# Performance work log

Hardware: AMD Instinct MI355X
Metric: run time of the kernel (lower is better)

The kernel has to match this reference:

```python
import jax, jax.numpy as jnp
import numpy as np

H = 64   # hidden_size
I = 4    # input_size
O = 1    # output_size

def setup_inputs() -> dict:
    key = jax.random.key(0)
    ks = jax.random.split(key, 7)
    B, T = 1024, 1024
    s = 1.0 / np.sqrt(H)
    x = jax.random.normal(ks[0], (B, T, I), dtype=jnp.float32)
    # PyTorch nn.LSTM params, gate order (i, f, g, o)
    W_ih = jax.random.uniform(ks[1], (4 * H, I), minval=-s, maxval=s, dtype=jnp.float32)
    W_hh = jax.random.uniform(ks[2], (4 * H, H), minval=-s, maxval=s, dtype=jnp.float32)
    b_ih = jax.random.uniform(ks[3], (4 * H,), minval=-s, maxval=s, dtype=jnp.float32)
    b_hh = jax.random.uniform(ks[4], (4 * H,), minval=-s, maxval=s, dtype=jnp.float32)
    W_fc = jax.random.uniform(ks[5], (O, H), minval=-s, maxval=s, dtype=jnp.float32)
    b_fc = jax.random.uniform(ks[6], (O,), minval=-s, maxval=s, dtype=jnp.float32)
    return {"x": x, "W_ih": W_ih, "W_hh": W_hh, "b_ih": b_ih, "b_hh": b_hh,
            "W_fc": W_fc, "b_fc": b_fc}

def _lstm(x, W_ih, W_hh, b_ih, b_hh):
    B, T, _ = x.shape
    # precompute input contribution for all timesteps: [T, B, 4H]
    xg = (jnp.einsum('bti,gi->btg', x, W_ih) + b_ih + b_hh).transpose(1, 0, 2)

    def step(carry, xt):
        h, c = carry
        g = xt + h @ W_hh.T                     # [B, 4H]
        i, f, gg, o = jnp.split(g, 4, axis=-1)  # torch gate order i,f,g,o
        i = jax.nn.sigmoid(i)
        f = jax.nn.sigmoid(f)
        gg = jnp.tanh(gg)
        o = jax.nn.sigmoid(o)
        c = f * c + i * gg
        h = o * jnp.tanh(c)
        return (h, c), h

    h0 = jnp.zeros((B, H), dtype=x.dtype)
    c0 = jnp.zeros((B, H), dtype=x.dtype)
    _, hs = jax.lax.scan(step, (h0, c0), xg)    # hs: [T, B, H]
    return hs.transpose(1, 0, 2)                # [B, T, H]

def reference(x, W_ih, W_hh, b_ih, b_hh, W_fc, b_fc):
    out = _lstm(x, W_ih, W_hh, b_ih, b_hh)      # [B, T, H]
    # dropout in eval mode == identity (deterministic reference)
    return out @ W_fc.T + b_fc                  # [B, T, 1]
```

## Files before the change

### kernel.cpp

```cpp
#include <hip/hip_runtime.h>

#define TLEN  1024
#define HN    64
#define LOG2E 1.4426950408889634f

typedef __fp16 half2v __attribute__((ext_vector_type(2)));
typedef __fp16 half8v __attribute__((ext_vector_type(8)));
typedef float  float4v __attribute__((ext_vector_type(4)));


#define FOR16(X) \
    X(0) X(1) X(2) X(3) X(4) X(5) X(6) X(7) \
    X(8) X(9) X(10) X(11) X(12) X(13) X(14) X(15)

__global__ __launch_bounds__(64, 1)
void lstm_mfma2(const float* __restrict__ x,
                const float* __restrict__ W_ih,
                const float* __restrict__ W_hh,
                const float* __restrict__ b_ih,
                const float* __restrict__ b_hh,
                const float* __restrict__ W_fc,
                const float* __restrict__ b_fc,
                float* __restrict__ out)
{
    const int b   = blockIdx.x;
    const int l   = threadIdx.x;
    const int col = l & 15;
    const int rg  = l >> 4;

    __shared__ float ring[64][65];
    __shared__ alignas(16) unsigned short hbuf[HN];

    hbuf[l] = 0;

#define DECLW(t) half8v wb##t##_0, wb##t##_1;
    FOR16(DECLW)
#undef DECLW

#define LOADW(t) { \
    const float sc = (((t) >> 2) == 2) ? (2.0f * LOG2E) : LOG2E; \
    const float* wr = W_hh + ((t) * 16 + col) * HN + rg * 8; \
    wb##t##_0[0] = (__fp16)(wr[0] * sc);  wb##t##_0[1] = (__fp16)(wr[1] * sc); \
    wb##t##_0[2] = (__fp16)(wr[2] * sc);  wb##t##_0[3] = (__fp16)(wr[3] * sc); \
    wb##t##_0[4] = (__fp16)(wr[4] * sc);  wb##t##_0[5] = (__fp16)(wr[5] * sc); \
    wb##t##_0[6] = (__fp16)(wr[6] * sc);  wb##t##_0[7] = (__fp16)(wr[7] * sc); \
    wb##t##_1[0] = (__fp16)(wr[32] * sc); wb##t##_1[1] = (__fp16)(wr[33] * sc); \
    wb##t##_1[2] = (__fp16)(wr[34] * sc); wb##t##_1[3] = (__fp16)(wr[35] * sc); \
    wb##t##_1[4] = (__fp16)(wr[36] * sc); wb##t##_1[5] = (__fp16)(wr[37] * sc); \
    wb##t##_1[6] = (__fp16)(wr[38] * sc); wb##t##_1[7] = (__fp16)(wr[39] * sc); \
    asm volatile("" : "+v"(wb##t##_0), "+v"(wb##t##_1)); }
    FOR16(LOADW)
#undef LOADW

    half2v wip0 = __builtin_amdgcn_cvt_pkrtz(W_ih[(0 * HN + l) * 4 + 0] * LOG2E,
                                             W_ih[(0 * HN + l) * 4 + 1] * LOG2E);
    half2v wip1 = __builtin_amdgcn_cvt_pkrtz(W_ih[(0 * HN + l) * 4 + 2] * LOG2E,
                                             W_ih[(0 * HN + l) * 4 + 3] * LOG2E);
    half2v wfp0 = __builtin_amdgcn_cvt_pkrtz(W_ih[(1 * HN + l) * 4 + 0] * LOG2E,
                                             W_ih[(1 * HN + l) * 4 + 1] * LOG2E);
    half2v wfp1 = __builtin_amdgcn_cvt_pkrtz(W_ih[(1 * HN + l) * 4 + 2] * LOG2E,
                                             W_ih[(1 * HN + l) * 4 + 3] * LOG2E);
    half2v wgp0 = __builtin_amdgcn_cvt_pkrtz(W_ih[(2 * HN + l) * 4 + 0] * 2.0f * LOG2E,
                                             W_ih[(2 * HN + l) * 4 + 1] * 2.0f * LOG2E);
    half2v wgp1 = __builtin_amdgcn_cvt_pkrtz(W_ih[(2 * HN + l) * 4 + 2] * 2.0f * LOG2E,
                                             W_ih[(2 * HN + l) * 4 + 3] * 2.0f * LOG2E);
    half2v wop0 = __builtin_amdgcn_cvt_pkrtz(W_ih[(3 * HN + l) * 4 + 0] * LOG2E,
                                             W_ih[(3 * HN + l) * 4 + 1] * LOG2E);
    half2v wop1 = __builtin_amdgcn_cvt_pkrtz(W_ih[(3 * HN + l) * 4 + 2] * LOG2E,
                                             W_ih[(3 * HN + l) * 4 + 3] * LOG2E);

    const float bias_i = (b_ih[0 * HN + l] + b_hh[0 * HN + l]) * LOG2E;
    const float bias_f = (b_ih[1 * HN + l] + b_hh[1 * HN + l]) * LOG2E;
    const float bias_g = (b_ih[2 * HN + l] + b_hh[2 * HN + l]) * (2.0f * LOG2E);
    const float bias_o = (b_ih[3 * HN + l] + b_hh[3 * HN + l]) * LOG2E;
    const float wfc = W_fc[l];
    const float bfc = b_fc[0];

    const bool rb0 = (rg & 1) != 0;
    const bool rb1 = (rg & 2) != 0;

    const float* xb = x   + (size_t)b * TLEN * 4;
    float*       ob = out + (size_t)b * TLEN;

    float h = 0.0f, c = 0.0f;
    const float4v zf = {0.0f, 0.0f, 0.0f, 0.0f};

    float4 xcur = *(const float4*)(xb + (size_t)l * 4);

    for (int ci = 0; ci < TLEN / 64; ++ci) {
        const int cn = (ci < TLEN / 64 - 1) ? ci + 1 : ci;
        float4 xnext = *(const float4*)(xb + (size_t)(cn * 64 + l) * 4);

        const int xq0 = __builtin_bit_cast(int, __builtin_amdgcn_cvt_pkrtz(xcur.x, xcur.y));
        const int xq1 = __builtin_bit_cast(int, __builtin_amdgcn_cvt_pkrtz(xcur.z, xcur.w));

        for (int s = 0; s < 64; ++s) {
            const half8v a0 = *(const half8v*)&hbuf[rg * 8];
            const half8v a1 = *(const half8v*)&hbuf[32 + rg * 8];

            const int xi0 = __builtin_amdgcn_readlane(xq0, s);
            const int xi1 = __builtin_amdgcn_readlane(xq1, s);
            const half2v xh0 = __builtin_bit_cast(half2v, xi0);
            const half2v xh1 = __builtin_bit_cast(half2v, xi1);

            float ai = __builtin_amdgcn_fdot2(wip0, xh0, bias_i, false);
            float af = __builtin_amdgcn_fdot2(wfp0, xh0, bias_f, false);
            float ag = __builtin_amdgcn_fdot2(wgp0, xh0, bias_g, false);
            float ao = __builtin_amdgcn_fdot2(wop0, xh0, bias_o, false);
            ai = __builtin_amdgcn_fdot2(wip1, xh1, ai, false);
            af = __builtin_amdgcn_fdot2(wfp1, xh1, af, false);
            ag = __builtin_amdgcn_fdot2(wgp1, xh1, ag, false);
            ao = __builtin_amdgcn_fdot2(wop1, xh1, ao, false);

#define MM(t) \
            float4v d##t = __builtin_amdgcn_mfma_f32_16x16x32_f16(a0, wb##t##_0, zf, 0, 0, 0); \
            d##t = __builtin_amdgcn_mfma_f32_16x16x32_f16(a1, wb##t##_1, d##t, 0, 0, 0);
            FOR16(MM)
#undef MM

            {
                const float i01 = rb0 ? d1[0]  : d0[0];
                const float i23 = rb0 ? d3[0]  : d2[0];
                ai += rb1 ? i23 : i01;
                const float f01 = rb0 ? d5[0]  : d4[0];
                const float f23 = rb0 ? d7[0]  : d6[0];
                af += rb1 ? f23 : f01;
                const float g01 = rb0 ? d9[0]  : d8[0];
                const float g23 = rb0 ? d11[0] : d10[0];
                ag += rb1 ? g23 : g01;
                const float o01 = rb0 ? d13[0] : d12[0];
                const float o23 = rb0 ? d15[0] : d14[0];
                ao += rb1 ? o23 : o01;
            }

            float si = __builtin_amdgcn_rcpf(1.0f + __builtin_amdgcn_exp2f(-ai));
            float sf = __builtin_amdgcn_rcpf(1.0f + __builtin_amdgcn_exp2f(-af));
            float tg = 1.0f - 2.0f * __builtin_amdgcn_rcpf(
                                         1.0f + __builtin_amdgcn_exp2f(ag));
            float so = __builtin_amdgcn_rcpf(1.0f + __builtin_amdgcn_exp2f(-ao));

            c = sf * c + si * tg;
            float th = 1.0f - 2.0f * __builtin_amdgcn_rcpf(
                           1.0f + __builtin_amdgcn_exp2f(c * (2.0f * LOG2E)));
            h = so * th;

            const int hpk = __builtin_bit_cast(int,
                                __builtin_amdgcn_cvt_pkrtz(h, h));
            hbuf[l] = (unsigned short)(hpk & 0xffff);
            ring[s][l] = h * wfc;
        }

        __syncthreads();
        float s0 = 0.f, s1 = 0.f, s2 = 0.f, s3 = 0.f;
#pragma unroll
        for (int k = 0; k < HN; k += 4) {
            s0 += ring[l][k];
            s1 += ring[l][k + 1];
            s2 += ring[l][k + 2];
            s3 += ring[l][k + 3];
        }
        ob[ci * 64 + l] = (s0 + s1) + (s2 + s3) + bfc;

        xcur = xnext;
    }
}

extern "C" void kernel_launch(void* const* d_in, const int* in_sizes, int n_in,
                              void* d_out, int out_size, void* d_ws, size_t ws_size,
                              hipStream_t stream) {
    const float* x    = (const float*)d_in[0];
    const float* W_ih = (const float*)d_in[1];
    const float* W_hh = (const float*)d_in[2];
    const float* b_ih = (const float*)d_in[3];
    const float* b_hh = (const float*)d_in[4];
    const float* W_fc = (const float*)d_in[5];
    const float* b_fc = (const float*)d_in[6];
    float* out = (float*)d_out;

    const int B = in_sizes[0] / (TLEN * 4);
    lstm_mfma2<<<dim3(B), dim3(64), 0, stream>>>(
        x, W_ih, W_hh, b_ih, b_hh, W_fc, b_fc, out);
}
```

Baseline: 525.8 us.

## Split recurrent matvec between MFMA for i,f gates and VALU dot2 for g,o

Halves the per-step MFMA count by computing only the input and forget gate recurrent products with matrix instructions, while the cell and output gate products are done per lane with packed fp16 dot2 instructions over the whole hidden vector read from LDS. The goal is to overlap matrix-unit and vector-ALU work on the serial per-step critical path. In exchange it adds 64 extra VGPRs of packed weights, eight broadcast LDS reads per step and 64 dot2 instructions per lane per step.

```diff
diff --git a/kernel.cpp b/kernel.cpp
--- a/kernel.cpp
+++ b/kernel.cpp
@@ -9,19 +9,22 @@
 typedef float  float4v __attribute__((ext_vector_type(4)));
 
 
-#define FOR16(X) \
+#define FOR8(X)  X(0) X(1) X(2) X(3) X(4) X(5) X(6) X(7)
+#define FOR32(X) \
     X(0) X(1) X(2) X(3) X(4) X(5) X(6) X(7) \
-    X(8) X(9) X(10) X(11) X(12) X(13) X(14) X(15)
+    X(8) X(9) X(10) X(11) X(12) X(13) X(14) X(15) \
+    X(16) X(17) X(18) X(19) X(20) X(21) X(22) X(23) \
+    X(24) X(25) X(26) X(27) X(28) X(29) X(30) X(31)
 
 __global__ __launch_bounds__(64, 1)
-void lstm_mfma2(const float* __restrict__ x,
-                const float* __restrict__ W_ih,
-                const float* __restrict__ W_hh,
-                const float* __restrict__ b_ih,
-                const float* __restrict__ b_hh,
-                const float* __restrict__ W_fc,
-                const float* __restrict__ b_fc,
-                float* __restrict__ out)
+void lstm_dual(const float* __restrict__ x,
+               const float* __restrict__ W_ih,
+               const float* __restrict__ W_hh,
+               const float* __restrict__ b_ih,
+               const float* __restrict__ b_hh,
+               const float* __restrict__ W_fc,
+               const float* __restrict__ b_fc,
+               float* __restrict__ out)
 {
     const int b   = blockIdx.x;
     const int l   = threadIdx.x;
@@ -34,23 +37,36 @@
     hbuf[l] = 0;
 
 #define DECLW(t) half8v wb##t##_0, wb##t##_1;
-    FOR16(DECLW)
+    FOR8(DECLW)
 #undef DECLW
 
 #define LOADW(t) { \
-    const float sc = (((t) >> 2) == 2) ? (2.0f * LOG2E) : LOG2E; \
     const float* wr = W_hh + ((t) * 16 + col) * HN + rg * 8; \
-    wb##t##_0[0] = (__fp16)(wr[0] * sc);  wb##t##_0[1] = (__fp16)(wr[1] * sc); \
-    wb##t##_0[2] = (__fp16)(wr[2] * sc);  wb##t##_0[3] = (__fp16)(wr[3] * sc); \
-    wb##t##_0[4] = (__fp16)(wr[4] * sc);  wb##t##_0[5] = (__fp16)(wr[5] * sc); \
-    wb##t##_0[6] = (__fp16)(wr[6] * sc);  wb##t##_0[7] = (__fp16)(wr[7] * sc); \
-    wb##t##_1[0] = (__fp16)(wr[32] * sc); wb##t##_1[1] = (__fp16)(wr[33] * sc); \
-    wb##t##_1[2] = (__fp16)(wr[34] * sc); wb##t##_1[3] = (__fp16)(wr[35] * sc); \
-    wb##t##_1[4] = (__fp16)(wr[36] * sc); wb##t##_1[5] = (__fp16)(wr[37] * sc); \
-    wb##t##_1[6] = (__fp16)(wr[38] * sc); wb##t##_1[7] = (__fp16)(wr[39] * sc); \
+    wb##t##_0[0] = (__fp16)(wr[0] * LOG2E);  wb##t##_0[1] = (__fp16)(wr[1] * LOG2E); \
+    wb##t##_0[2] = (__fp16)(wr[2] * LOG2E);  wb##t##_0[3] = (__fp16)(wr[3] * LOG2E); \
+    wb##t##_0[4] = (__fp16)(wr[4] * LOG2E);  wb##t##_0[5] = (__fp16)(wr[5] * LOG2E); \
+    wb##t##_0[6] = (__fp16)(wr[6] * LOG2E);  wb##t##_0[7] = (__fp16)(wr[7] * LOG2E); \
+    wb##t##_1[0] = (__fp16)(wr[32] * LOG2E); wb##t##_1[1] = (__fp16)(wr[33] * LOG2E); \
+    wb##t##_1[2] = (__fp16)(wr[34] * LOG2E); wb##t##_1[3] = (__fp16)(wr[35] * LOG2E); \
+    wb##t##_1[4] = (__fp16)(wr[36] * LOG2E); wb##t##_1[5] = (__fp16)(wr[37] * LOG2E); \
+    wb##t##_1[6] = (__fp16)(wr[38] * LOG2E); wb##t##_1[7] = (__fp16)(wr[39] * LOG2E); \
     asm volatile("" : "+v"(wb##t##_0), "+v"(wb##t##_1)); }
-    FOR16(LOADW)
+    FOR8(LOADW)
 #undef LOADW
+
+    const float* wr_g = W_hh + (2 * HN + l) * HN;
+    const float* wr_o = W_hh + (3 * HN + l) * HN;
+#define DECLP(P) half2v pg##P, po##P;
+    FOR32(DECLP)
+#undef DECLP
+#define LOADP(P) \
+    pg##P = __builtin_amdgcn_cvt_pkrtz(wr_g[2 * (P)] * (2.0f * LOG2E), \
+                                       wr_g[2 * (P) + 1] * (2.0f * LOG2E)); \
+    po##P = __builtin_amdgcn_cvt_pkrtz(wr_o[2 * (P)] * LOG2E, \
+                                       wr_o[2 * (P) + 1] * LOG2E); \
+    asm volatile("" : "+v"(pg##P), "+v"(po##P));
+    FOR32(LOADP)
+#undef LOADP
 
     half2v wip0 = __builtin_amdgcn_cvt_pkrtz(W_ih[(0 * HN + l) * 4 + 0] * LOG2E,
                                              W_ih[(0 * HN + l) * 4 + 1] * LOG2E);
@@ -97,6 +113,20 @@
         for (int s = 0; s < 64; ++s) {
             const half8v a0 = *(const half8v*)&hbuf[rg * 8];
             const half8v a1 = *(const half8v*)&hbuf[32 + rg * 8];
+            const uint4 q0 = *(const uint4*)&hbuf[0];
+            const uint4 q1 = *(const uint4*)&hbuf[8];
+            const uint4 q2 = *(const uint4*)&hbuf[16];
+            const uint4 q3 = *(const uint4*)&hbuf[24];
+            const uint4 q4 = *(const uint4*)&hbuf[32];
+            const uint4 q5 = *(const uint4*)&hbuf[40];
+            const uint4 q6 = *(const uint4*)&hbuf[48];
+            const uint4 q7 = *(const uint4*)&hbuf[56];
+
+#define MM(t) \
+            float4v d##t = __builtin_amdgcn_mfma_f32_16x16x32_f16(a0, wb##t##_0, zf, 0, 0, 0); \
+            d##t = __builtin_amdgcn_mfma_f32_16x16x32_f16(a1, wb##t##_1, d##t, 0, 0, 0);
+            FOR8(MM)
+#undef MM
 
             const int xi0 = __builtin_amdgcn_readlane(xq0, s);
             const int xi1 = __builtin_amdgcn_readlane(xq1, s);
@@ -105,32 +135,46 @@
 
             float ai = __builtin_amdgcn_fdot2(wip0, xh0, bias_i, false);
             float af = __builtin_amdgcn_fdot2(wfp0, xh0, bias_f, false);
-            float ag = __builtin_amdgcn_fdot2(wgp0, xh0, bias_g, false);
-            float ao = __builtin_amdgcn_fdot2(wop0, xh0, bias_o, false);
+            float agE = __builtin_amdgcn_fdot2(wgp0, xh0, bias_g, false);
+            float aoE = __builtin_amdgcn_fdot2(wop0, xh0, bias_o, false);
             ai = __builtin_amdgcn_fdot2(wip1, xh1, ai, false);
             af = __builtin_amdgcn_fdot2(wfp1, xh1, af, false);
-            ag = __builtin_amdgcn_fdot2(wgp1, xh1, ag, false);
-            ao = __builtin_amdgcn_fdot2(wop1, xh1, ao, false);
-
-#define MM(t) \
-            float4v d##t = __builtin_amdgcn_mfma_f32_16x16x32_f16(a0, wb##t##_0, zf, 0, 0, 0); \
-            d##t = __builtin_amdgcn_mfma_f32_16x16x32_f16(a1, wb##t##_1, d##t, 0, 0, 0);
-            FOR16(MM)
-#undef MM
+            agE = __builtin_amdgcn_fdot2(wgp1, xh1, agE, false);
+            aoE = __builtin_amdgcn_fdot2(wop1, xh1, aoE, false);
+            float agO = 0.0f, aoO = 0.0f;
+
+#define GOB(q, P0, P1, P2, P3, AG, AO) { \
+            const half2v hA = __builtin_bit_cast(half2v, (int)(q).x); \
+            const half2v hB = __builtin_bit_cast(half2v, (int)(q).y); \
+            const half2v hC = __builtin_bit_cast(half2v, (int)(q).z); \
+            const half2v hD = __builtin_bit_cast(half2v, (int)(q).w); \
+            AG = __builtin_amdgcn_fdot2(pg##P0, hA, AG, false); \
+            AO = __builtin_amdgcn_fdot2(po##P0, hA, AO, false); \
+            AG = __builtin_amdgcn_fdot2(pg##P1, hB, AG, false); \
+            AO = __builtin_amdgcn_fdot2(po##P1, hB, AO, false); \
+            AG = __builtin_amdgcn_fdot2(pg##P2, hC, AG, false); \
+            AO = __builtin_amdgcn_fdot2(po##P2, hC, AO, false); \
+            AG = __builtin_amdgcn_fdot2(pg##P3, hD, AG, false); \
+            AO = __builtin_amdgcn_fdot2(po##P3, hD, AO, false); }
+            GOB(q0, 0, 1, 2, 3,     agE, aoE)
+            GOB(q4, 16, 17, 18, 19, agO, aoO)
+            GOB(q1, 4, 5, 6, 7,     agE, aoE)
+            GOB(q5, 20, 21, 22, 23, agO, aoO)
+            GOB(q2, 8, 9, 10, 11,   agE, aoE)
+            GOB(q6, 24, 25, 26, 27, agO, aoO)
+            GOB(q3, 12, 13, 14, 15, agE, aoE)
+            GOB(q7, 28, 29, 30, 31, agO, aoO)
+#undef GOB
+            const float ag = agE + agO;
+            const float ao = aoE + aoO;
 
             {
-                const float i01 = rb0 ? d1[0]  : d0[0];
-                const float i23 = rb0 ? d3[0]  : d2[0];
+                const float i01 = rb0 ? d1[0] : d0[0];
+                const float i23 = rb0 ? d3[0] : d2[0];
                 ai += rb1 ? i23 : i01;
-                const float f01 = rb0 ? d5[0]  : d4[0];
-                const float f23 = rb0 ? d7[0]  : d6[0];
+                const float f01 = rb0 ? d5[0] : d4[0];
+                const float f23 = rb0 ? d7[0] : d6[0];
                 af += rb1 ? f23 : f01;
-                const float g01 = rb0 ? d9[0]  : d8[0];
-                const float g23 = rb0 ? d11[0] : d10[0];
-                ag += rb1 ? g23 : g01;
-                const float o01 = rb0 ? d13[0] : d12[0];
-                const float o23 = rb0 ? d15[0] : d14[0];
-                ao += rb1 ? o23 : o01;
             }
 
             float si = __builtin_amdgcn_rcpf(1.0f + __builtin_amdgcn_exp2f(-ai));
@@ -178,6 +222,6 @@
     float* out = (float*)d_out;
 
     const int B = in_sizes[0] / (TLEN * 4);
-    lstm_mfma2<<<dim3(B), dim3(64), 0, stream>>>(
+    lstm_dual<<<dim3(B), dim3(64), 0, stream>>>(
         x, W_ih, W_hh, b_ih, b_hh, W_fc, b_fc, out);
 }
```

New measurement: 596.9 us. 1.14x slower.

## Pack four batch sequences per wavefront using distinct MFMA rows

Applied to the files above, without the earlier changes.

Each 64-lane block now processes four batch elements instead of one. Each element's hidden state sits in its own group of MFMA A-matrix rows, so the recurrent matmul no longer repeats the same row 16 times. Each lane now computes gates and cell state for four hidden units, and the input projection is staged through shared memory per 16-step chunk. The output reduction is rewritten for the new layout and gets an extra barrier. The grid shrinks fourfold, which cuts total MFMA work but puts four times the activation math on each step's serial path. It may also leave many SIMDs idle.

```diff
diff --git a/kernel.cpp b/kernel.cpp
--- a/kernel.cpp
+++ b/kernel.cpp
@@ -12,31 +12,32 @@
 #define FOR16(X) \
     X(0) X(1) X(2) X(3) X(4) X(5) X(6) X(7) \
     X(8) X(9) X(10) X(11) X(12) X(13) X(14) X(15)
+#define FORC(X) X(0) X(1) X(2) X(3)
 
 __global__ __launch_bounds__(64, 1)
-void lstm_mfma2(const float* __restrict__ x,
-                const float* __restrict__ W_ih,
-                const float* __restrict__ W_hh,
-                const float* __restrict__ b_ih,
-                const float* __restrict__ b_hh,
-                const float* __restrict__ W_fc,
-                const float* __restrict__ b_fc,
-                float* __restrict__ out)
+void lstm_e4(const float* __restrict__ x,
+             const float* __restrict__ W_ih,
+             const float* __restrict__ W_hh,
+             const float* __restrict__ b_ih,
+             const float* __restrict__ b_hh,
+             const float* __restrict__ W_fc,
+             const float* __restrict__ b_fc,
+             float* __restrict__ out)
 {
-    const int b   = blockIdx.x;
+    const int b0  = blockIdx.x * 4;
     const int l   = threadIdx.x;
     const int col = l & 15;
     const int rg  = l >> 4;
 
-    __shared__ float ring[64][65];
-    __shared__ alignas(16) unsigned short hbuf[HN];
+    __shared__ alignas(16) unsigned short hbuf[4 * 88];
+    __shared__ alignas(16) unsigned int   xbuf[4 * 34];
+    __shared__ alignas(16) float          ring[16 * 80];
 
-    hbuf[l] = 0;
+    for (int i = l; i < 4 * 88; i += 64) hbuf[i] = 0;
 
 #define DECLW(t) half8v wb##t##_0, wb##t##_1;
     FOR16(DECLW)
 #undef DECLW
-
 #define LOADW(t) { \
     const float sc = (((t) >> 2) == 2) ? (2.0f * LOG2E) : LOG2E; \
     const float* wr = W_hh + ((t) * 16 + col) * HN + rg * 8; \
@@ -52,114 +53,112 @@
     FOR16(LOADW)
 #undef LOADW
 
-    half2v wip0 = __builtin_amdgcn_cvt_pkrtz(W_ih[(0 * HN + l) * 4 + 0] * LOG2E,
-                                             W_ih[(0 * HN + l) * 4 + 1] * LOG2E);
-    half2v wip1 = __builtin_amdgcn_cvt_pkrtz(W_ih[(0 * HN + l) * 4 + 2] * LOG2E,
-                                             W_ih[(0 * HN + l) * 4 + 3] * LOG2E);
-    half2v wfp0 = __builtin_amdgcn_cvt_pkrtz(W_ih[(1 * HN + l) * 4 + 0] * LOG2E,
-                                             W_ih[(1 * HN + l) * 4 + 1] * LOG2E);
-    half2v wfp1 = __builtin_amdgcn_cvt_pkrtz(W_ih[(1 * HN + l) * 4 + 2] * LOG2E,
-                                             W_ih[(1 * HN + l) * 4 + 3] * LOG2E);
-    half2v wgp0 = __builtin_amdgcn_cvt_pkrtz(W_ih[(2 * HN + l) * 4 + 0] * 2.0f * LOG2E,
-                                             W_ih[(2 * HN + l) * 4 + 1] * 2.0f * LOG2E);
-    half2v wgp1 = __builtin_amdgcn_cvt_pkrtz(W_ih[(2 * HN + l) * 4 + 2] * 2.0f * LOG2E,
-                                             W_ih[(2 * HN + l) * 4 + 3] * 2.0f * LOG2E);
-    half2v wop0 = __builtin_amdgcn_cvt_pkrtz(W_ih[(3 * HN + l) * 4 + 0] * LOG2E,
-                                             W_ih[(3 * HN + l) * 4 + 1] * LOG2E);
-    half2v wop1 = __builtin_amdgcn_cvt_pkrtz(W_ih[(3 * HN + l) * 4 + 2] * LOG2E,
-                                             W_ih[(3 * HN + l) * 4 + 3] * LOG2E);
+#define DECLX(c) \
+    half2v wxi##c##a, wxi##c##b, wxf##c##a, wxf##c##b; \
+    half2v wxg##c##a, wxg##c##b, wxo##c##a, wxo##c##b; \
+    float bi##c, bf##c, bg##c, bo##c, wq##c; float cst##c = 0.0f;
+    FORC(DECLX)
+#undef DECLX
+#define LOADX(c) { \
+    const int u = (c) * 16 + col; \
+    wxi##c##a = __builtin_amdgcn_cvt_pkrtz(W_ih[(0*HN+u)*4+0]*LOG2E, W_ih[(0*HN+u)*4+1]*LOG2E); \
+    wxi##c##b = __builtin_amdgcn_cvt_pkrtz(W_ih[(0*HN+u)*4+2]*LOG2E, W_ih[(0*HN+u)*4+3]*LOG2E); \
+    wxf##c##a = __builtin_amdgcn_cvt_pkrtz(W_ih[(1*HN+u)*4+0]*LOG2E, W_ih[(1*HN+u)*4+1]*LOG2E); \
+    wxf##c##b = __builtin_amdgcn_cvt_pkrtz(W_ih[(1*HN+u)*4+2]*LOG2E, W_ih[(1*HN+u)*4+3]*LOG2E); \
+    wxg##c##a = __builtin_amdgcn_cvt_pkrtz(W_ih[(2*HN+u)*4+0]*2.0f*LOG2E, W_ih[(2*HN+u)*4+1]*2.0f*LOG2E); \
+    wxg##c##b = __builtin_amdgcn_cvt_pkrtz(W_ih[(2*HN+u)*4+2]*2.0f*LOG2E, W_ih[(2*HN+u)*4+3]*2.0f*LOG2E); \
+    wxo##c##a = __builtin_amdgcn_cvt_pkrtz(W_ih[(3*HN+u)*4+0]*LOG2E, W_ih[(3*HN+u)*4+1]*LOG2E); \
+    wxo##c##b = __builtin_amdgcn_cvt_pkrtz(W_ih[(3*HN+u)*4+2]*LOG2E, W_ih[(3*HN+u)*4+3]*LOG2E); \
+    bi##c = (b_ih[0*HN+u] + b_hh[0*HN+u]) * LOG2E; \
+    bf##c = (b_ih[1*HN+u] + b_hh[1*HN+u]) * LOG2E; \
+    bg##c = (b_ih[2*HN+u] + b_hh[2*HN+u]) * (2.0f*LOG2E); \
+    bo##c = (b_ih[3*HN+u] + b_hh[3*HN+u]) * LOG2E; \
+    wq##c = W_fc[u]; }
+    FORC(LOADX)
+#undef LOADX
 
-    const float bias_i = (b_ih[0 * HN + l] + b_hh[0 * HN + l]) * LOG2E;
-    const float bias_f = (b_ih[1 * HN + l] + b_hh[1 * HN + l]) * LOG2E;
-    const float bias_g = (b_ih[2 * HN + l] + b_hh[2 * HN + l]) * (2.0f * LOG2E);
-    const float bias_o = (b_ih[3 * HN + l] + b_hh[3 * HN + l]) * LOG2E;
-    const float wfc = W_fc[l];
     const float bfc = b_fc[0];
+    const int   ea  = col >> 2;
 
-    const bool rb0 = (rg & 1) != 0;
-    const bool rb1 = (rg & 2) != 0;
+    float4 xcur = *(const float4*)(x + ((size_t)(b0 + rg) * TLEN + col) * 4);
 
-    const float* xb = x   + (size_t)b * TLEN * 4;
-    float*       ob = out + (size_t)b * TLEN;
+    for (int ci = 0; ci < TLEN / 16; ++ci) {
+        const unsigned xi0 = (unsigned)__builtin_bit_cast(int,
+                                 __builtin_amdgcn_cvt_pkrtz(xcur.x, xcur.y));
+        const unsigned xi1 = (unsigned)__builtin_bit_cast(int,
+                                 __builtin_amdgcn_cvt_pkrtz(xcur.z, xcur.w));
+        *(uint2*)&xbuf[rg * 34 + col * 2] = make_uint2(xi0, xi1);
 
-    float h = 0.0f, c = 0.0f;
-    const float4v zf = {0.0f, 0.0f, 0.0f, 0.0f};
+        const int cn = (ci < TLEN / 16 - 1) ? ci + 1 : ci;
+        float4 xnext = *(const float4*)(x + ((size_t)(b0 + rg) * TLEN
+                                             + cn * 16 + col) * 4);
 
-    float4 xcur = *(const float4*)(xb + (size_t)l * 4);
+        for (int s = 0; s < 16; ++s) {
+            const half8v a0 = *(const half8v*)&hbuf[ea * 88 + rg * 8];
+            const half8v a1 = *(const half8v*)&hbuf[ea * 88 + 32 + rg * 8];
+            const uint2 xw = *(const uint2*)&xbuf[rg * 34 + s * 2];
+            const half2v xh0 = __builtin_bit_cast(half2v, (int)xw.x);
+            const half2v xh1 = __builtin_bit_cast(half2v, (int)xw.y);
 
-    for (int ci = 0; ci < TLEN / 64; ++ci) {
-        const int cn = (ci < TLEN / 64 - 1) ? ci + 1 : ci;
-        float4 xnext = *(const float4*)(xb + (size_t)(cn * 64 + l) * 4);
+#define XDOT(c) \
+            float ai##c = __builtin_amdgcn_fdot2(wxi##c##a, xh0, bi##c, false); \
+            float af##c = __builtin_amdgcn_fdot2(wxf##c##a, xh0, bf##c, false); \
+            float ag##c = __builtin_amdgcn_fdot2(wxg##c##a, xh0, bg##c, false); \
+            float ao##c = __builtin_amdgcn_fdot2(wxo##c##a, xh0, bo##c, false); \
+            ai##c = __builtin_amdgcn_fdot2(wxi##c##b, xh1, ai##c, false); \
+            af##c = __builtin_amdgcn_fdot2(wxf##c##b, xh1, af##c, false); \
+            ag##c = __builtin_amdgcn_fdot2(wxg##c##b, xh1, ag##c, false); \
+            ao##c = __builtin_amdgcn_fdot2(wxo##c##b, xh1, ao##c, false);
+            FORC(XDOT)
+#undef XDOT
 
-        const int xq0 = __builtin_bit_cast(int, __builtin_amdgcn_cvt_pkrtz(xcur.x, xcur.y));
-        const int xq1 = __builtin_bit_cast(int, __builtin_amdgcn_cvt_pkrtz(xcur.z, xcur.w));
-
-        for (int s = 0; s < 64; ++s) {
-            const half8v a0 = *(const half8v*)&hbuf[rg * 8];
-            const half8v a1 = *(const half8v*)&hbuf[32 + rg * 8];
-
-            const int xi0 = __builtin_amdgcn_readlane(xq0, s);
-            const int xi1 = __builtin_amdgcn_readlane(xq1, s);
-            const half2v xh0 = __builtin_bit_cast(half2v, xi0);
-            const half2v xh1 = __builtin_bit_cast(half2v, xi1);
-
-            float ai = __builtin_amdgcn_fdot2(wip0, xh0, bias_i, false);
-            float af = __builtin_amdgcn_fdot2(wfp0, xh0, bias_f, false);
-            float ag = __builtin_amdgcn_fdot2(wgp0, xh0, bias_g, false);
-            float ao = __builtin_amdgcn_fdot2(wop0, xh0, bias_o, false);
-            ai = __builtin_amdgcn_fdot2(wip1, xh1, ai, false);
-            af = __builtin_amdgcn_fdot2(wfp1, xh1, af, false);
-            ag = __builtin_amdgcn_fdot2(wgp1, xh1, ag, false);
-            ao = __builtin_amdgcn_fdot2(wop1, xh1, ao, false);
-
+            const float4v zf = {0.0f, 0.0f, 0.0f, 0.0f};
 #define MM(t) \
             float4v d##t = __builtin_amdgcn_mfma_f32_16x16x32_f16(a0, wb##t##_0, zf, 0, 0, 0); \
             d##t = __builtin_amdgcn_mfma_f32_16x16x32_f16(a1, wb##t##_1, d##t, 0, 0, 0);
             FOR16(MM)
 #undef MM
+            ai0 += d0[0];  ai1 += d1[0];  ai2 += d2[0];  ai3 += d3[0];
+            af0 += d4[0];  af1 += d5[0];  af2 += d6[0];  af3 += d7[0];
+            ag0 += d8[0];  ag1 += d9[0];  ag2 += d10[0]; ag3 += d11[0];
+            ao0 += d12[0]; ao1 += d13[0]; ao2 += d14[0]; ao3 += d15[0];
 
-            {
-                const float i01 = rb0 ? d1[0]  : d0[0];
-                const float i23 = rb0 ? d3[0]  : d2[0];
-                ai += rb1 ? i23 : i01;
-                const float f01 = rb0 ? d5[0]  : d4[0];
-                const float f23 = rb0 ? d7[0]  : d6[0];
-                af += rb1 ? f23 : f01;
-                const float g01 = rb0 ? d9[0]  : d8[0];
-                const float g23 = rb0 ? d11[0] : d10[0];
-                ag += rb1 ? g23 : g01;
-                const float o01 = rb0 ? d13[0] : d12[0];
-                const float o23 = rb0 ? d15[0] : d14[0];
-                ao += rb1 ? o23 : o01;
-            }
+#define ACT(c) \
+            const float si##c = __builtin_amdgcn_rcpf(1.0f + __builtin_amdgcn_exp2f(-ai##c)); \
+            const float sf##c = __builtin_amdgcn_rcpf(1.0f + __builtin_amdgcn_exp2f(-af##c)); \
+            const float tg##c = 1.0f - 2.0f * __builtin_amdgcn_rcpf(1.0f + __builtin_amdgcn_exp2f(ag##c)); \
+            const float so##c = __builtin_amdgcn_rcpf(1.0f + __builtin_amdgcn_exp2f(-ao##c)); \
+            cst##c = sf##c * cst##c + si##c * tg##c; \
+            const float th##c = 1.0f - 2.0f * __builtin_amdgcn_rcpf( \
+                1.0f + __builtin_amdgcn_exp2f(cst##c * (2.0f * LOG2E))); \
+            const float h##c = so##c * th##c;
+            FORC(ACT)
+#undef ACT
 
-            float si = __builtin_amdgcn_rcpf(1.0f + __builtin_amdgcn_exp2f(-ai));
-            float sf = __builtin_amdgcn_rcpf(1.0f + __builtin_amdgcn_exp2f(-af));
-            float tg = 1.0f - 2.0f * __builtin_amdgcn_rcpf(
-                                         1.0f + __builtin_amdgcn_exp2f(ag));
-            float so = __builtin_amdgcn_rcpf(1.0f + __builtin_amdgcn_exp2f(-ao));
+#define PUB(c) hbuf[rg * 88 + (c) * 16 + col] = (unsigned short) \
+            (__builtin_bit_cast(int, __builtin_amdgcn_cvt_pkrtz(h##c, h##c)) & 0xffff);
+            FORC(PUB)
+#undef PUB
 
-            c = sf * c + si * tg;
-            float th = 1.0f - 2.0f * __builtin_amdgcn_rcpf(
-                           1.0f + __builtin_amdgcn_exp2f(c * (2.0f * LOG2E)));
-            h = so * th;
-
-            const int hpk = __builtin_bit_cast(int,
-                                __builtin_amdgcn_cvt_pkrtz(h, h));
-            hbuf[l] = (unsigned short)(hpk & 0xffff);
-            ring[s][l] = h * wfc;
+            ring[s * 80 + rg * 20 + col] =
+                (h0 * wq0 + h1 * wq1) + (h2 * wq2 + h3 * wq3);
         }
 
         __syncthreads();
-        float s0 = 0.f, s1 = 0.f, s2 = 0.f, s3 = 0.f;
-#pragma unroll
-        for (int k = 0; k < HN; k += 4) {
-            s0 += ring[l][k];
-            s1 += ring[l][k + 1];
-            s2 += ring[l][k + 2];
-            s3 += ring[l][k + 3];
+        {
+            const int e2 = l >> 4, s2 = l & 15;
+            const float* rb = &ring[s2 * 80 + e2 * 20];
+            const float4 r0 = *(const float4*)&rb[0];
+            const float4 r1 = *(const float4*)&rb[4];
+            const float4 r2 = *(const float4*)&rb[8];
+            const float4 r3 = *(const float4*)&rb[12];
+            const float sum = ((r0.x + r0.y) + (r0.z + r0.w))
+                            + ((r1.x + r1.y) + (r1.z + r1.w))
+                            + ((r2.x + r2.y) + (r2.z + r2.w))
+                            + ((r3.x + r3.y) + (r3.z + r3.w));
+            out[(size_t)(b0 + e2) * TLEN + ci * 16 + s2] = sum + bfc;
         }
-        ob[ci * 64 + l] = (s0 + s1) + (s2 + s3) + bfc;
+        __syncthreads();
 
         xcur = xnext;
     }
@@ -178,6 +177,6 @@
     float* out = (float*)d_out;
 
     const int B = in_sizes[0] / (TLEN * 4);
-    lstm_mfma2<<<dim3(B), dim3(64), 0, stream>>>(
+    lstm_e4<<<dim3(B / 4), dim3(64), 0, stream>>>(
         x, W_ih, W_hh, b_ih, b_hh, W_fc, b_fc, out);
 }
```

Result: slower. 830.1 us (+57.9%).
